# Kernel optimization log

Measured on AMD Instinct MI355X. Metric: run time of the kernel, lower is better.

## Reference

```python
import math
import jax, jax.numpy as jnp
import numpy as np

B, T, D = 2, 2048, 2048
NH, HD = 16, 48           # query heads, head dim
LAT, NLH = 256, 8         # latent dim, latent (kv) heads
EPS = 1e-5


def setup_inputs() -> dict:
    key = jax.random.key(0)
    ks = jax.random.split(key, 7)
    x = jax.random.normal(ks[0], (B, T, D), dtype=jnp.float32)
    # causal mask [B, 1, T, T]
    mask = jnp.broadcast_to(jnp.tril(jnp.ones((T, T), dtype=bool))[None, None], (B, 1, T, T))
    s = lambda fan_in: 1.0 / math.sqrt(fan_in)
    Wq = jax.random.normal(ks[1], (D, NH * HD), dtype=jnp.float32) * s(D)
    Wkv = jax.random.normal(ks[2], (D, LAT), dtype=jnp.float32) * s(D)
    w_norm = jnp.ones((LAT,), dtype=jnp.float32)
    Wk = jax.random.normal(ks[3], (LAT, NLH * HD), dtype=jnp.float32) * s(LAT)
    Wv = jax.random.normal(ks[4], (LAT, NLH * HD), dtype=jnp.float32) * s(LAT)
    Wo = jax.random.normal(ks[5], (NH * HD, D), dtype=jnp.float32) * s(NH * HD)
    return {"x": x, "mask": mask, "Wq": Wq, "Wkv": Wkv, "w_norm": w_norm,
            "Wk": Wk, "Wv": Wv, "Wo": Wo}


def rms_norm(x, weight, eps=EPS):
    var = jnp.mean(x * x, axis=-1, keepdims=True)
    return x * jax.lax.rsqrt(var + eps) * weight


def reference(x, mask, Wq, Wkv, w_norm, Wk, Wv, Wo):
    b, t, _ = x.shape
    q = (x @ Wq).reshape(b, t, NH, HD)                      # [B,T,NH,HD]
    kv_latent = rms_norm(x @ Wkv, w_norm)                   # [B,T,LAT]
    k = (kv_latent @ Wk).reshape(b, t, NLH, HD)             # [B,T,NLH,HD]
    v = (kv_latent @ Wv).reshape(b, t, NLH, HD)
    rep = NH // NLH
    k = jnp.repeat(k, rep, axis=2)                          # [B,T,NH,HD]
    v = jnp.repeat(v, rep, axis=2)
    q = q.transpose(0, 2, 1, 3)                             # [B,NH,T,HD]
    k = k.transpose(0, 2, 1, 3)
    v = v.transpose(0, 2, 1, 3)
    scale = 1.0 / math.sqrt(HD)
    scores = jnp.einsum('bhqd,bhkd->bhqk', q, k) * scale    # [B,NH,T,T]
    scores = jnp.where(mask, scores, -1e9)
    attn = jax.nn.softmax(scores, axis=-1)
    out = jnp.einsum('bhqk,bhkd->bhqd', attn, v)            # [B,NH,T,HD]
    out = out.transpose(0, 2, 1, 3).reshape(b, t, NH * HD)
    return out @ Wo                                          # [B,T,D]
```

## Files before the change

kernel.cpp:

```cpp
#include <hip/hip_runtime.h>
#include <hip/hip_bf16.h>

typedef __hip_bfloat16 bf16;
typedef __attribute__((ext_vector_type(8))) short short8;
typedef __attribute__((ext_vector_type(4))) float f32x4;

#define Bq   2
#define Tq   2048
#define Dq   2048
#define NHq  16
#define HDq  48
#define LATq 256
#define NLHq 8
#define QN   (NHq * HDq)
#define KVN  (NLHq * HDq)

__device__ __forceinline__ unsigned short f2u(float x) {
    __hip_bfloat16 h = __float2bfloat16(x);
    return *reinterpret_cast<unsigned short*>(&h);
}
__device__ __forceinline__ float u2f(unsigned short u) {
    return __uint_as_float((unsigned)u << 16);
}
__device__ __forceinline__ unsigned pk2(float a, float b) {
    return (unsigned)f2u(a) | ((unsigned)f2u(b) << 16);
}

__global__ void __launch_bounds__(256)
cvt_x(const float* __restrict__ in, bf16* __restrict__ out) {
    const size_t i = ((size_t)blockIdx.x * 256 + threadIdx.x) * 8;
    const float4 a = *(const float4*)&in[i];
    const float4 b = *(const float4*)&in[i + 4];
    uint4 u;
    u.x = pk2(a.x, a.y); u.y = pk2(a.z, a.w);
    u.z = pk2(b.x, b.y); u.w = pk2(b.z, b.w);
    *(uint4*)&out[i] = u;
}

__global__ void __launch_bounds__(256)
tr_w(const float* __restrict__ W, bf16* __restrict__ WT, int K, int N) {
    __shared__ float ts[32][33];
    const int n0 = blockIdx.x * 32, k0 = blockIdx.y * 32;
    const int t = threadIdx.x;
    const int r = t >> 3, c4 = (t & 7) * 4;
    const float4 v = *(const float4*)&W[(size_t)(k0 + r) * N + n0 + c4];
    ts[r][c4] = v.x; ts[r][c4 + 1] = v.y; ts[r][c4 + 2] = v.z; ts[r][c4 + 3] = v.w;
    __syncthreads();
    const unsigned u0 = pk2(ts[c4][r], ts[c4 + 1][r]);
    const unsigned u1 = pk2(ts[c4 + 2][r], ts[c4 + 3][r]);
    *(uint2*)&WT[(size_t)(n0 + r) * K + k0 + c4] = make_uint2(u0, u1);
}

template<int MODE>
__global__ void __launch_bounds__(256)
gemm128(const bf16* __restrict__ A, const bf16* __restrict__ BT,
        void* __restrict__ C0v, void* __restrict__ C1v, int K) {
    __shared__ short As[2][128 * 40];
    __shared__ short Bs[2][64 * 40];
    const int t  = threadIdx.x;
    const int m0 = blockIdx.x * 128;
    const int n0 = blockIdx.y * 64;
    const int w  = t >> 6;
    const int wm = (w & 1) * 64;
    const int wn = (w >> 1) * 32;
    const int lr = t & 15;
    const int quad = (t >> 4) & 3;
    const int sr = t >> 2, sc = t & 3;

    f32x4 acc[4][2];
    #pragma unroll
    for (int mi = 0; mi < 4; ++mi)
        #pragma unroll
        for (int ni = 0; ni < 2; ++ni) acc[mi][ni] = (f32x4){0.f, 0.f, 0.f, 0.f};

    int aoff[4], boff[2];
    #pragma unroll
    for (int mi = 0; mi < 4; ++mi) aoff[mi] = (wm + mi * 16 + lr) * 40 + quad * 8;
    #pragma unroll
    for (int ni = 0; ni < 2; ++ni) boff[ni] = (wn + ni * 16 + lr) * 40 + quad * 8;

    uint4 pa0, pa1, pb0;
    auto glo = [&](int kt) {
        const int kb = kt * 32 + sc * 8;
        pa0 = *(const uint4*)&A[(size_t)(m0 + sr) * K + kb];
        pa1 = *(const uint4*)&A[(size_t)(m0 + 64 + sr) * K + kb];
        pb0 = *(const uint4*)&BT[(size_t)(n0 + sr) * K + kb];
    };
    auto lwrite = [&](int bb) {
        *(uint4*)&As[bb][sr * 40 + sc * 8] = pa0;
        *(uint4*)&As[bb][(64 + sr) * 40 + sc * 8] = pa1;
        *(uint4*)&Bs[bb][sr * 40 + sc * 8] = pb0;
    };

    const int nk = K / 32;
    glo(0);
    lwrite(0);
    __syncthreads();
    int cur = 0;

    for (int kt = 0; kt < nk; ++kt) {
        const bool pref = (kt + 1 < nk);
        if (pref) glo(kt + 1);
        short8 af[4], bfr[2];
        #pragma unroll
        for (int mi = 0; mi < 4; ++mi) af[mi] = *(const short8*)&As[cur][aoff[mi]];
        #pragma unroll
        for (int ni = 0; ni < 2; ++ni) bfr[ni] = *(const short8*)&Bs[cur][boff[ni]];
        #pragma unroll
        for (int mi = 0; mi < 4; ++mi)
            #pragma unroll
            for (int ni = 0; ni < 2; ++ni)
                acc[mi][ni] = __builtin_amdgcn_mfma_f32_16x16x32_bf16(af[mi], bfr[ni], acc[mi][ni], 0, 0, 0);
        if (pref) lwrite(cur ^ 1);
        __syncthreads();
        cur ^= 1;
    }

    #pragma unroll
    for (int mi = 0; mi < 4; ++mi)
        #pragma unroll
        for (int ni = 0; ni < 2; ++ni) {
            const int col = n0 + wn + ni * 16 + lr;
            #pragma unroll
            for (int r = 0; r < 4; ++r) {
                const int row = m0 + wm + mi * 16 + quad * 4 + r;
                const float v = acc[mi][ni][r];
                if constexpr (MODE == 0) {
                    if (col < QN) ((bf16*)C0v)[(size_t)row * QN + col] = __float2bfloat16(v);
                    else ((float*)C1v)[(size_t)row * LATq + (col - QN)] = v;
                } else if constexpr (MODE == 1) {
                    if (col < KVN) ((bf16*)C0v)[(size_t)row * KVN + col] = __float2bfloat16(v);
                    else ((bf16*)C1v)[(size_t)row * KVN + (col - KVN)] = __float2bfloat16(v);
                } else {
                    ((float*)C0v)[(size_t)row * Dq + col] = v;
                }
            }
        }
}

__global__ void __launch_bounds__(256)
mla_kvrms(const float* __restrict__ xkv, const float* __restrict__ wn,
          bf16* __restrict__ lat) {
    const int t = threadIdx.x;
    const int row = blockIdx.x * 4 + (t >> 6);
    const int lane = t & 63;
    const float4 v = *(const float4*)&xkv[(size_t)row * LATq + lane * 4];
    float ss = v.x * v.x + v.y * v.y + v.z * v.z + v.w * v.w;
    ss += __shfl_xor(ss, 1);  ss += __shfl_xor(ss, 2);  ss += __shfl_xor(ss, 4);
    ss += __shfl_xor(ss, 8);  ss += __shfl_xor(ss, 16); ss += __shfl_xor(ss, 32);
    const float rr = rsqrtf(ss * (1.0f / LATq) + 1e-5f);
    const float4 g = *(const float4*)&wn[lane * 4];
    const unsigned w0 = pk2(v.x * rr * g.x, v.y * rr * g.y);
    const unsigned w1 = pk2(v.z * rr * g.z, v.w * rr * g.w);
    *(uint2*)&lat[(size_t)row * LATq + lane * 4] = make_uint2(w0, w1);
}

__global__ void __launch_bounds__(256)
mla_attn(const bf16* __restrict__ q, const bf16* __restrict__ kk,
         const bf16* __restrict__ vv, bf16* __restrict__ ao) {
    __shared__ __align__(16) short Ks[2][64 * 48];
    __shared__ __align__(16) short Vt[2][48 * 72];
    __shared__ __align__(16) short Ps[4][2 * 16 * 72];
    const int t    = threadIdx.x;
    const int g    = blockIdx.x;
    const int qy   = blockIdx.y;
    const int b    = blockIdx.z;
    const int qt0  = (qy < 16) ? (qy << 1) : (63 - (qy << 1));
    const int qt   = b ? (31 - qt0) : qt0;
    const int w    = t >> 6;
    const int lane = t & 63;
    const int lr   = t & 15;
    const int quad = (t >> 4) & 3;
    const int hh   = w & 1;
    const int rh   = w >> 1;
    const int h    = g * 2 + hh;
    const int Q0   = qt * 64;
    const float scale = 0.14433756729740643f;
    const short8 z8 = {0, 0, 0, 0, 0, 0, 0, 0};

    short8 qf[2][2];
    int qg[2];
    #pragma unroll
    for (int st = 0; st < 2; ++st) {
        qg[st] = Q0 + rh * 32 + st * 16 + lr;
        const bf16* qr = q + (size_t)(b * Tq + qg[st]) * QN + h * HDq;
        qf[st][0] = *(const short8*)(qr + quad * 8);
        const short8 q1 = *(const short8*)(qr + 32 + (quad & 1) * 8);
        qf[st][1] = (quad < 2) ? q1 : z8;
    }

    const bf16* kb = kk + (size_t)b * Tq * KVN + g * HDq;
    const bf16* vb = vv + (size_t)b * Tq * KVN + g * HDq;

    float m[2] = {-1e30f, -1e30f}, l[2] = {0.f, 0.f};
    f32x4 acc[2][3];
    #pragma unroll
    for (int st = 0; st < 2; ++st)
        #pragma unroll
        for (int dm = 0; dm < 3; ++dm) acc[st][dm] = (f32x4){0.f, 0.f, 0.f, 0.f};

    short* Pw = &Ps[w][0];
    uint4 pre[3];

    auto issue = [&](int tl) {
        #pragma unroll
        for (int r = 0; r < 3; ++r) {
            if (w < 2) {
                const int idx = (w * 3 + r) * 64 + lane;
                const int row = idx / 6, ch = idx - row * 6;
                pre[r] = *(const uint4*)(kb + (size_t)(tl * 64 + row) * KVN + ch * 8);
            } else {
                const int idx = ((w - 2) * 3 + r) * 64 + lane;
                const int kp = idx & 31, hc = idx >> 5;
                const bf16* src = vb + (size_t)(tl * 64 + 2 * kp) * KVN + hc * 4;
                const uint2 a2 = *(const uint2*)src;
                const uint2 b2 = *(const uint2*)(src + KVN);
                pre[r].x = a2.x; pre[r].y = a2.y; pre[r].z = b2.x; pre[r].w = b2.y;
            }
        }
    };
    auto lwrite = [&](int bb) {
        #pragma unroll
        for (int r = 0; r < 3; ++r) {
            if (w < 2) {
                const int idx = (w * 3 + r) * 64 + lane;
                const int row = idx / 6, ch = idx - row * 6;
                *(uint4*)&Ks[bb][row * 48 + ch * 8] = pre[r];
            } else {
                const int idx = ((w - 2) * 3 + r) * 64 + lane;
                const int kp = idx & 31, hc = idx >> 5;
                const unsigned short* u = (const unsigned short*)&pre[r];
                #pragma unroll
                for (int j = 0; j < 4; ++j)
                    *(unsigned*)&Vt[bb][(hc * 4 + j) * 72 + 2 * kp] =
                        (unsigned)u[j] | ((unsigned)u[4 + j] << 16);
            }
        }
    };

    issue(0);
    lwrite(0);
    __syncthreads();
    int cur = 0;

    for (int tl = 0; tl <= qt; ++tl) {
        const bool pref = (tl < qt);
        if (pref) issue(tl + 1);

        f32x4 sc[2][4];
        #pragma unroll
        for (int mt = 0; mt < 4; ++mt) {
            const short8 k0 = *(const short8*)&Ks[cur][(mt * 16 + lr) * 48 + quad * 8];
            const short8 k1v = *(const short8*)&Ks[cur][(mt * 16 + lr) * 48 + 32 + (quad & 1) * 8];
            const short8 k1 = (quad < 2) ? k1v : z8;
            #pragma unroll
            for (int st = 0; st < 2; ++st) {
                f32x4 s = (f32x4){0.f, 0.f, 0.f, 0.f};
                s = __builtin_amdgcn_mfma_f32_16x16x32_bf16(k0, qf[st][0], s, 0, 0, 0);
                s = __builtin_amdgcn_mfma_f32_16x16x32_bf16(k1, qf[st][1], s, 0, 0, 0);
                sc[st][mt] = s;
            }
        }
        if (tl == qt) {
            #pragma unroll
            for (int st = 0; st < 2; ++st) {
                const int qloc = rh * 32 + st * 16 + lr;
                #pragma unroll
                for (int mt = 0; mt < 4; ++mt)
                    #pragma unroll
                    for (int r = 0; r < 4; ++r)
                        if (mt * 16 + quad * 4 + r > qloc) sc[st][mt][r] = -1e30f;
            }
        }
        #pragma unroll
        for (int st = 0; st < 2; ++st) {
            float mx = -1e30f;
            #pragma unroll
            for (int mt = 0; mt < 4; ++mt)
                #pragma unroll
                for (int r = 0; r < 4; ++r) mx = fmaxf(mx, sc[st][mt][r]);
            mx = fmaxf(mx, __shfl_xor(mx, 16));
            mx = fmaxf(mx, __shfl_xor(mx, 32));
            const float mn = fmaxf(m[st], mx * scale);
            const float f  = __expf(m[st] - mn);
            m[st] = mn;
            float rs = 0.f;
            #pragma unroll
            for (int mt = 0; mt < 4; ++mt)
                #pragma unroll
                for (int r = 0; r < 4; ++r) {
                    const float p = u2f(f2u(__expf(fmaf(sc[st][mt][r], scale, -mn))));
                    sc[st][mt][r] = p;
                    rs += p;
                }
            rs += __shfl_xor(rs, 16);
            rs += __shfl_xor(rs, 32);
            l[st] = l[st] * f + rs;
            #pragma unroll
            for (int dm = 0; dm < 3; ++dm)
                #pragma unroll
                for (int r = 0; r < 4; ++r) acc[st][dm][r] *= f;
            short* Pst = Pw + st * 16 * 72;
            #pragma unroll
            for (int mt = 0; mt < 4; ++mt) {
                unsigned* pw = (unsigned*)&Pst[lr * 72 + mt * 16 + quad * 4];
                pw[0] = pk2(sc[st][mt][0], sc[st][mt][1]);
                pw[1] = pk2(sc[st][mt][2], sc[st][mt][3]);
            }
        }
        short8 pf[2][2];
        #pragma unroll
        for (int st = 0; st < 2; ++st) {
            const short* Pst = Pw + st * 16 * 72;
            pf[st][0] = *(const short8*)&Pst[lr * 72 + quad * 8];
            pf[st][1] = *(const short8*)&Pst[lr * 72 + 32 + quad * 8];
        }
        #pragma unroll
        for (int dm = 0; dm < 3; ++dm) {
            const short8 v0 = *(const short8*)&Vt[cur][(dm * 16 + lr) * 72 + quad * 8];
            const short8 v1 = *(const short8*)&Vt[cur][(dm * 16 + lr) * 72 + 32 + quad * 8];
            #pragma unroll
            for (int st = 0; st < 2; ++st) {
                acc[st][dm] = __builtin_amdgcn_mfma_f32_16x16x32_bf16(v0, pf[st][0], acc[st][dm], 0, 0, 0);
                acc[st][dm] = __builtin_amdgcn_mfma_f32_16x16x32_bf16(v1, pf[st][1], acc[st][dm], 0, 0, 0);
            }
        }

        if (pref) lwrite(cur ^ 1);
        __syncthreads();
        cur ^= 1;
    }

    #pragma unroll
    for (int st = 0; st < 2; ++st) {
        const float inv = 1.0f / l[st];
        bf16* orow = ao + (size_t)(b * Tq + qg[st]) * QN + h * HDq;
        #pragma unroll
        for (int dm = 0; dm < 3; ++dm) {
            const unsigned w0 = pk2(acc[st][dm][0] * inv, acc[st][dm][1] * inv);
            const unsigned w1 = pk2(acc[st][dm][2] * inv, acc[st][dm][3] * inv);
            *(uint2*)(orow + dm * 16 + quad * 4) = make_uint2(w0, w1);
        }
    }
}

extern "C" void kernel_launch(void* const* d_in, const int* in_sizes, int n_in,
                              void* d_out, int out_size, void* d_ws, size_t ws_size,
                              hipStream_t stream) {
    const float* x   = (const float*)d_in[0];
    const float* Wq  = (const float*)d_in[2];
    const float* Wkv = (const float*)d_in[3];
    const float* wn  = (const float*)d_in[4];
    const float* Wk  = (const float*)d_in[5];
    const float* Wv  = (const float*)d_in[6];
    const float* Wo  = (const float*)d_in[7];
    float* out = (float*)d_out;

    const int M = Bq * Tq;
    char* ob = (char*)d_out;
    bf16*  xb    = (bf16*)ob;
    bf16*  qws   = (bf16*)(ob + 16777216);
    float* xkv   = (float*)(ob + 23068672);
    bf16*  latb  = (bf16*)(ob + 27262976);
    bf16*  WqkvT = (bf16*)(ob + 29360128);
    bf16*  WkvpT = (bf16*)ob;
    bf16*  kws = (bf16*)d_ws;
    bf16*  vws = kws + (size_t)M * KVN;
    bf16*  aob = vws + (size_t)M * KVN;
    bf16*  WoT = (bf16*)d_ws;

    cvt_x <<<4096, 256, 0, stream>>>(x, xb);
    tr_w  <<<dim3(QN / 32, Dq / 32), 256, 0, stream>>>(Wq, WqkvT, Dq, QN);
    tr_w  <<<dim3(LATq / 32, Dq / 32), 256, 0, stream>>>(Wkv, WqkvT + (size_t)QN * Dq, Dq, LATq);
    gemm128<0> <<<dim3(M / 128, 1024 / 64), 256, 0, stream>>>(xb, WqkvT, qws, xkv, Dq);
    tr_w  <<<dim3(KVN / 32, LATq / 32), 256, 0, stream>>>(Wk, WkvpT, LATq, KVN);
    tr_w  <<<dim3(KVN / 32, LATq / 32), 256, 0, stream>>>(Wv, WkvpT + (size_t)KVN * LATq, LATq, KVN);
    mla_kvrms <<<M / 4, 256, 0, stream>>>(xkv, wn, latb);
    gemm128<1> <<<dim3(M / 128, 768 / 64), 256, 0, stream>>>(latb, WkvpT, kws, vws, LATq);
    mla_attn <<<dim3(NLHq, 32, Bq), 256, 0, stream>>>(qws, kws, vws, aob);
    tr_w  <<<dim3(Dq / 32, QN / 32), 256, 0, stream>>>(Wo, WoT, QN, Dq);
    gemm128<2> <<<dim3(M / 128, Dq / 64), 256, 0, stream>>>(aob, WoT, out, nullptr, QN);
}
```

Before: 279.4 us.

## Split attention query tile across two blocks to double grid size

Each attention block now handles 32 query rows instead of 64: each wave owns one 16-row slice rather than two, and the grid doubles along the query axis. This raises the number of blocks from 512 to 1024 and shrinks per-thread registers and P shared memory, aiming at better occupancy and CU fill on the large GPU. In exchange each K/V tile is loaded from global memory and staged through LDS twice as often, once per half-block, so K/V traffic and sync overhead per query row increase.

```diff
diff --git a/kernel.cpp b/kernel.cpp
--- a/kernel.cpp
+++ b/kernel.cpp
@@ -160,12 +160,14 @@
          const bf16* __restrict__ vv, bf16* __restrict__ ao) {
     __shared__ __align__(16) short Ks[2][64 * 48];
     __shared__ __align__(16) short Vt[2][48 * 72];
-    __shared__ __align__(16) short Ps[4][2 * 16 * 72];
+    __shared__ __align__(16) short Ps[4][16 * 72];
     const int t    = threadIdx.x;
     const int g    = blockIdx.x;
     const int qy   = blockIdx.y;
     const int b    = blockIdx.z;
-    const int qt0  = (qy < 16) ? (qy << 1) : (63 - (qy << 1));
+    const int u    = qy >> 1;
+    const int half = (qy & 1) * 32;
+    const int qt0  = (u < 16) ? (u << 1) : (63 - (u << 1));
     const int qt   = b ? (31 - qt0) : qt0;
     const int w    = t >> 6;
     const int lane = t & 63;
@@ -174,30 +176,23 @@
     const int hh   = w & 1;
     const int rh   = w >> 1;
     const int h    = g * 2 + hh;
-    const int Q0   = qt * 64;
     const float scale = 0.14433756729740643f;
     const short8 z8 = {0, 0, 0, 0, 0, 0, 0, 0};
 
-    short8 qf[2][2];
-    int qg[2];
-    #pragma unroll
-    for (int st = 0; st < 2; ++st) {
-        qg[st] = Q0 + rh * 32 + st * 16 + lr;
-        const bf16* qr = q + (size_t)(b * Tq + qg[st]) * QN + h * HDq;
-        qf[st][0] = *(const short8*)(qr + quad * 8);
-        const short8 q1 = *(const short8*)(qr + 32 + (quad & 1) * 8);
-        qf[st][1] = (quad < 2) ? q1 : z8;
-    }
+    const int qloc = half + rh * 16 + lr;
+    const int qg   = qt * 64 + qloc;
+    const bf16* qr = q + (size_t)(b * Tq + qg) * QN + h * HDq;
+    short8 qf0 = *(const short8*)(qr + quad * 8);
+    const short8 q1 = *(const short8*)(qr + 32 + (quad & 1) * 8);
+    short8 qf1 = (quad < 2) ? q1 : z8;
 
     const bf16* kb = kk + (size_t)b * Tq * KVN + g * HDq;
     const bf16* vb = vv + (size_t)b * Tq * KVN + g * HDq;
 
-    float m[2] = {-1e30f, -1e30f}, l[2] = {0.f, 0.f};
-    f32x4 acc[2][3];
-    #pragma unroll
-    for (int st = 0; st < 2; ++st)
-        #pragma unroll
-        for (int dm = 0; dm < 3; ++dm) acc[st][dm] = (f32x4){0.f, 0.f, 0.f, 0.f};
+    float m = -1e30f, l = 0.f;
+    f32x4 acc[3];
+    #pragma unroll
+    for (int dm = 0; dm < 3; ++dm) acc[dm] = (f32x4){0.f, 0.f, 0.f, 0.f};
 
     short* Pw = &Ps[w][0];
     uint4 pre[3];
@@ -229,11 +224,11 @@
             } else {
                 const int idx = ((w - 2) * 3 + r) * 64 + lane;
                 const int kp = idx & 31, hc = idx >> 5;
-                const unsigned short* u = (const unsigned short*)&pre[r];
+                const unsigned short* uu = (const unsigned short*)&pre[r];
                 #pragma unroll
                 for (int j = 0; j < 4; ++j)
                     *(unsigned*)&Vt[bb][(hc * 4 + j) * 72 + 2 * kp] =
-                        (unsigned)u[j] | ((unsigned)u[4 + j] << 16);
+                        (unsigned)uu[j] | ((unsigned)uu[4 + j] << 16);
             }
         }
     };
@@ -247,83 +242,64 @@
         const bool pref = (tl < qt);
         if (pref) issue(tl + 1);
 
-        f32x4 sc[2][4];
+        f32x4 sc[4];
         #pragma unroll
         for (int mt = 0; mt < 4; ++mt) {
             const short8 k0 = *(const short8*)&Ks[cur][(mt * 16 + lr) * 48 + quad * 8];
             const short8 k1v = *(const short8*)&Ks[cur][(mt * 16 + lr) * 48 + 32 + (quad & 1) * 8];
             const short8 k1 = (quad < 2) ? k1v : z8;
-            #pragma unroll
-            for (int st = 0; st < 2; ++st) {
-                f32x4 s = (f32x4){0.f, 0.f, 0.f, 0.f};
-                s = __builtin_amdgcn_mfma_f32_16x16x32_bf16(k0, qf[st][0], s, 0, 0, 0);
-                s = __builtin_amdgcn_mfma_f32_16x16x32_bf16(k1, qf[st][1], s, 0, 0, 0);
-                sc[st][mt] = s;
-            }
+            f32x4 s = (f32x4){0.f, 0.f, 0.f, 0.f};
+            s = __builtin_amdgcn_mfma_f32_16x16x32_bf16(k0, qf0, s, 0, 0, 0);
+            s = __builtin_amdgcn_mfma_f32_16x16x32_bf16(k1, qf1, s, 0, 0, 0);
+            sc[mt] = s;
         }
         if (tl == qt) {
-            #pragma unroll
-            for (int st = 0; st < 2; ++st) {
-                const int qloc = rh * 32 + st * 16 + lr;
-                #pragma unroll
-                for (int mt = 0; mt < 4; ++mt)
-                    #pragma unroll
-                    for (int r = 0; r < 4; ++r)
-                        if (mt * 16 + quad * 4 + r > qloc) sc[st][mt][r] = -1e30f;
-            }
-        }
-        #pragma unroll
-        for (int st = 0; st < 2; ++st) {
-            float mx = -1e30f;
             #pragma unroll
             for (int mt = 0; mt < 4; ++mt)
                 #pragma unroll
-                for (int r = 0; r < 4; ++r) mx = fmaxf(mx, sc[st][mt][r]);
-            mx = fmaxf(mx, __shfl_xor(mx, 16));
-            mx = fmaxf(mx, __shfl_xor(mx, 32));
-            const float mn = fmaxf(m[st], mx * scale);
-            const float f  = __expf(m[st] - mn);
-            m[st] = mn;
-            float rs = 0.f;
-            #pragma unroll
-            for (int mt = 0; mt < 4; ++mt)
-                #pragma unroll
-                for (int r = 0; r < 4; ++r) {
-                    const float p = u2f(f2u(__expf(fmaf(sc[st][mt][r], scale, -mn))));
-                    sc[st][mt][r] = p;
-                    rs += p;
-                }
-            rs += __shfl_xor(rs, 16);
-            rs += __shfl_xor(rs, 32);
-            l[st] = l[st] * f + rs;
-            #pragma unroll
-            for (int dm = 0; dm < 3; ++dm)
-                #pragma unroll
-                for (int r = 0; r < 4; ++r) acc[st][dm][r] *= f;
-            short* Pst = Pw + st * 16 * 72;
-            #pragma unroll
-            for (int mt = 0; mt < 4; ++mt) {
-                unsigned* pw = (unsigned*)&Pst[lr * 72 + mt * 16 + quad * 4];
-                pw[0] = pk2(sc[st][mt][0], sc[st][mt][1]);
-                pw[1] = pk2(sc[st][mt][2], sc[st][mt][3]);
+                for (int r = 0; r < 4; ++r)
+                    if (mt * 16 + quad * 4 + r > qloc) sc[mt][r] = -1e30f;
+        }
+        float mx = -1e30f;
+        #pragma unroll
+        for (int mt = 0; mt < 4; ++mt)
+            #pragma unroll
+            for (int r = 0; r < 4; ++r) mx = fmaxf(mx, sc[mt][r]);
+        mx = fmaxf(mx, __shfl_xor(mx, 16));
+        mx = fmaxf(mx, __shfl_xor(mx, 32));
+        const float mn = fmaxf(m, mx * scale);
+        const float f  = __expf(m - mn);
+        m = mn;
+        float rs = 0.f;
+        #pragma unroll
+        for (int mt = 0; mt < 4; ++mt)
+            #pragma unroll
+            for (int r = 0; r < 4; ++r) {
+                const float p = u2f(f2u(__expf(fmaf(sc[mt][r], scale, -mn))));
+                sc[mt][r] = p;
+                rs += p;
             }
-        }
-        short8 pf[2][2];
-        #pragma unroll
-        for (int st = 0; st < 2; ++st) {
-            const short* Pst = Pw + st * 16 * 72;
-            pf[st][0] = *(const short8*)&Pst[lr * 72 + quad * 8];
-            pf[st][1] = *(const short8*)&Pst[lr * 72 + 32 + quad * 8];
-        }
+        rs += __shfl_xor(rs, 16);
+        rs += __shfl_xor(rs, 32);
+        l = l * f + rs;
+        #pragma unroll
+        for (int dm = 0; dm < 3; ++dm)
+            #pragma unroll
+            for (int r = 0; r < 4; ++r) acc[dm][r] *= f;
+        #pragma unroll
+        for (int mt = 0; mt < 4; ++mt) {
+            unsigned* pw = (unsigned*)&Pw[lr * 72 + mt * 16 + quad * 4];
+            pw[0] = pk2(sc[mt][0], sc[mt][1]);
+            pw[1] = pk2(sc[mt][2], sc[mt][3]);
+        }
+        const short8 pf0 = *(const short8*)&Pw[lr * 72 + quad * 8];
+        const short8 pf1 = *(const short8*)&Pw[lr * 72 + 32 + quad * 8];
         #pragma unroll
         for (int dm = 0; dm < 3; ++dm) {
             const short8 v0 = *(const short8*)&Vt[cur][(dm * 16 + lr) * 72 + quad * 8];
             const short8 v1 = *(const short8*)&Vt[cur][(dm * 16 + lr) * 72 + 32 + quad * 8];
-            #pragma unroll
-            for (int st = 0; st < 2; ++st) {
-                acc[st][dm] = __builtin_amdgcn_mfma_f32_16x16x32_bf16(v0, pf[st][0], acc[st][dm], 0, 0, 0);
-                acc[st][dm] = __builtin_amdgcn_mfma_f32_16x16x32_bf16(v1, pf[st][1], acc[st][dm], 0, 0, 0);
-            }
+            acc[dm] = __builtin_amdgcn_mfma_f32_16x16x32_bf16(v0, pf0, acc[dm], 0, 0, 0);
+            acc[dm] = __builtin_amdgcn_mfma_f32_16x16x32_bf16(v1, pf1, acc[dm], 0, 0, 0);
         }
 
         if (pref) lwrite(cur ^ 1);
@@ -331,16 +307,13 @@
         cur ^= 1;
     }
 
-    #pragma unroll
-    for (int st = 0; st < 2; ++st) {
-        const float inv = 1.0f / l[st];
-        bf16* orow = ao + (size_t)(b * Tq + qg[st]) * QN + h * HDq;
-        #pragma unroll
-        for (int dm = 0; dm < 3; ++dm) {
-            const unsigned w0 = pk2(acc[st][dm][0] * inv, acc[st][dm][1] * inv);
-            const unsigned w1 = pk2(acc[st][dm][2] * inv, acc[st][dm][3] * inv);
-            *(uint2*)(orow + dm * 16 + quad * 4) = make_uint2(w0, w1);
-        }
+    const float inv = 1.0f / l;
+    bf16* orow = ao + (size_t)(b * Tq + qg) * QN + h * HDq;
+    #pragma unroll
+    for (int dm = 0; dm < 3; ++dm) {
+        const unsigned w0 = pk2(acc[dm][0] * inv, acc[dm][1] * inv);
+        const unsigned w1 = pk2(acc[dm][2] * inv, acc[dm][3] * inv);
+        *(uint2*)(orow + dm * 16 + quad * 4) = make_uint2(w0, w1);
     }
 }
 
@@ -377,7 +350,7 @@
     tr_w  <<<dim3(KVN / 32, LATq / 32), 256, 0, stream>>>(Wv, WkvpT + (size_t)KVN * LATq, LATq, KVN);
     mla_kvrms <<<M / 4, 256, 0, stream>>>(xkv, wn, latb);
     gemm128<1> <<<dim3(M / 128, 768 / 64), 256, 0, stream>>>(latb, WkvpT, kws, vws, LATq);
-    mla_attn <<<dim3(NLHq, 32, Bq), 256, 0, stream>>>(qws, kws, vws, aob);
+    mla_attn <<<dim3(NLHq, 64, Bq), 256, 0, stream>>>(qws, kws, vws, aob);
     tr_w  <<<dim3(Dq / 32, QN / 32), 256, 0, stream>>>(Wo, WoT, QN, Dq);
     gemm128<2> <<<dim3(M / 128, Dq / 64), 256, 0, stream>>>(aob, WoT, out, nullptr, QN);
 }
```

Result: slower. 289.4 us (+3.6%).
